# Performance work log

Measured on AMD Instinct MI355X. Metric: run time of the kernel, lower is better.

The kernel has to match this reference:

```python
import jax, jax.numpy as jnp
import numpy as np

DIM_IN1 = 512
DIM_IN2 = 512
DIM_OUT = 64


def setup_inputs() -> dict:
    key = jax.random.key(0)
    k1, k2, kw, kb = jax.random.split(key, 4)
    B, L = 8, 256
    inputs1 = jax.random.normal(k1, (B, L, DIM_IN1), dtype=jnp.float32)
    inputs2 = jax.random.normal(k2, (B, L, DIM_IN2), dtype=jnp.float32)
    # nn.Bilinear init: U(-1/sqrt(in1_features), 1/sqrt(in1_features))
    bound = 1.0 / np.sqrt(DIM_IN1)
    weight = jax.random.uniform(kw, (DIM_OUT, DIM_IN1, DIM_IN2), dtype=jnp.float32,
                                minval=-bound, maxval=bound)
    bias = jax.random.uniform(kb, (DIM_OUT,), dtype=jnp.float32,
                              minval=-bound, maxval=bound)
    return {"inputs1": inputs1, "inputs2": inputs2, "weight": weight, "bias": bias}


def reference(inputs1, inputs2, weight, bias):
    # out[b,i,j,k] = sum_{p,q} x1[b,i,p] * W[k,p,q] * x2[b,j,q] + bias[k]
    # Two smaller batched matmuls instead of materializing [B,L,L,D] expansions.
    tmp = jnp.einsum('bip,kpq->bikq', inputs1, weight)   # [B, L, K, D2]
    out = jnp.einsum('bikq,bjq->bijk', tmp, inputs2)      # [B, L, L, K]
    return out + bias
```

## Files before the change

kernel.cpp:

```cpp
#include <hip/hip_runtime.h>
#include <hip/hip_bf16.h>
#include <stdint.h>


typedef __bf16 bf16x8 __attribute__((ext_vector_type(8)));
typedef float  f32x4  __attribute__((ext_vector_type(4)));

#define BM 128
#define BN 128
#define BK 64
#define LDSK 72
#define KDIM 512

__global__ __launch_bounds__(256) void f32_to_bf16_kernel(
    const float* __restrict__ in, __bf16* __restrict__ out, long n8)
{
    for (long i = blockIdx.x * 256L + threadIdx.x; i < n8; i += gridDim.x * 256L) {
        f32x4 a = *(const f32x4*)(in + i * 8);
        f32x4 b = *(const f32x4*)(in + i * 8 + 4);
        bf16x8 o;
        o[0]=(__bf16)a[0]; o[1]=(__bf16)a[1]; o[2]=(__bf16)a[2]; o[3]=(__bf16)a[3];
        o[4]=(__bf16)b[0]; o[5]=(__bf16)b[1]; o[6]=(__bf16)b[2]; o[7]=(__bf16)b[3];
        *(bf16x8*)(out + i * 8) = o;
    }
}

template <typename OutT>
__global__ __launch_bounds__(256) void gemm_nt_bf16(
    const __bf16* __restrict__ A,
    const __bf16* __restrict__ B,
    OutT* __restrict__ C,
    const float* __restrict__ bias,
    int ldc,
    long sA, long sB, long sC)
{
    const int tid  = threadIdx.x;
    const int lane = tid & 63;
    const int wave = tid >> 6;
    const int wm = wave & 1;
    const int wn = wave >> 1;
    const long z = blockIdx.z;
    A += z * sA;  B += z * sB;  C += z * sC;

    const int m0 = blockIdx.y * BM;
    const int n0 = blockIdx.x * BN;

    __shared__ __bf16 sAt[BM * LDSK];
    __shared__ __bf16 sBt[BN * LDSK];

    f32x4 acc[4][4] = {};

    const int krow = lane >> 4;
    const int lcol = lane & 15;

    const int srow = tid >> 3;
    const int skc  = tid & 7;

    for (int kt = 0; kt < KDIM / BK; ++kt) {
        const __bf16* gA = A + (long)m0 * KDIM + kt * BK;
        const __bf16* gB = B + (long)n0 * KDIM + kt * BK;
#pragma unroll
        for (int it = 0; it < 4; ++it) {
            int row = it * 32 + srow;
            *(bf16x8*)&sAt[row * LDSK + skc * 8] =
                *(const bf16x8*)(gA + (long)row * KDIM + skc * 8);
        }
#pragma unroll
        for (int it = 0; it < 4; ++it) {
            int row = it * 32 + srow;
            *(bf16x8*)&sBt[row * LDSK + skc * 8] =
                *(const bf16x8*)(gB + (long)row * KDIM + skc * 8);
        }
        __syncthreads();
#pragma unroll
        for (int kk = 0; kk < BK / 32; ++kk) {
            bf16x8 af[4], bfr[4];
#pragma unroll
            for (int i = 0; i < 4; ++i)
                af[i] = *(const bf16x8*)&sAt[(wm * 64 + i * 16 + lcol) * LDSK + kk * 32 + krow * 8];
#pragma unroll
            for (int j = 0; j < 4; ++j)
                bfr[j] = *(const bf16x8*)&sBt[(wn * 64 + j * 16 + lcol) * LDSK + kk * 32 + krow * 8];
#pragma unroll
            for (int i = 0; i < 4; ++i)
#pragma unroll
                for (int j = 0; j < 4; ++j)
                    acc[i][j] = __builtin_amdgcn_mfma_f32_16x16x32_bf16(af[i], bfr[j], acc[i][j], 0, 0, 0);
        }
        __syncthreads();
    }

#pragma unroll
    for (int j = 0; j < 4; ++j) {
        const int col = n0 + wn * 64 + j * 16 + lcol;
        float badd = bias ? bias[col & 63] : 0.f;
#pragma unroll
        for (int i = 0; i < 4; ++i) {
            const int rowb = m0 + wm * 64 + i * 16 + krow * 4;
#pragma unroll
            for (int r = 0; r < 4; ++r) {
                float v = acc[i][j][r] + badd;
                C[(long)(rowb + r) * ldc + col] = (OutT)v;
            }
        }
    }
}

extern "C" void kernel_launch(void* const* d_in, const int* in_sizes, int n_in,
                              void* d_out, int out_size, void* d_ws, size_t ws_size,
                              hipStream_t stream)
{
    (void)in_sizes; (void)n_in; (void)out_size;
    const float* x1f = (const float*)d_in[0];
    const float* x2f = (const float*)d_in[1];
    const float* Wf  = (const float*)d_in[2];
    const float* bs  = (const float*)d_in[3];
    float* out = (float*)d_out;

    const long N_W = 64L * 512 * 512;
    const long N_X = 8L * 256 * 512;
    __bf16* Wb  = (__bf16*)d_ws;
    __bf16* x1b = Wb + N_W;
    __bf16* x2b = x1b + N_X;
    __bf16* S   = x2b + N_X;
    const size_t head_bytes = (size_t)(N_W + 2 * N_X) * sizeof(__bf16);

    f32_to_bf16_kernel<<<2048, 256, 0, stream>>>(Wf,  Wb,  N_W / 8);
    f32_to_bf16_kernel<<<512,  256, 0, stream>>>(x1f, x1b, N_X / 8);
    f32_to_bf16_kernel<<<512,  256, 0, stream>>>(x2f, x2b, N_X / 8);

    const long ROWS_TOTAL = 2048;
    const long ROW_ELEMS  = 32768;

    long rows_chunk = (ws_size > head_bytes)
        ? (long)((ws_size - head_bytes) / (ROW_ELEMS * sizeof(__bf16))) : 0;
    rows_chunk &= ~255L;
    if (rows_chunk < 256) rows_chunk = 256;
    if (rows_chunk > ROWS_TOTAL) rows_chunk = ROWS_TOTAL;

    for (long r0 = 0; r0 < ROWS_TOTAL; r0 += rows_chunk) {
        long rows = ROWS_TOTAL - r0;
        if (rows > rows_chunk) rows = rows_chunk;
        long nbc = rows >> 8;

        dim3 gA(32768 / BN, (unsigned)(rows / BM), 1);
        gemm_nt_bf16<__bf16><<<gA, 256, 0, stream>>>(
            x2b + r0 * KDIM, Wb, S, nullptr, 32768, 0, 0, 0);

        dim3 gB(16384 / BN, 256 / BM, (unsigned)nbc);
        gemm_nt_bf16<float><<<gB, 256, 0, stream>>>(
            x1b + r0 * KDIM,
            S,
            out + r0 * 16384,
            bs, 16384,
            256L * KDIM,
            256L * ROW_ELEMS,
            256L * 16384);
    }
}
```

Baseline: 345.3 us.

## Use 256x256 tiles with double-buffered swizzled LDS and XCD-aware block remap

Replaces the 128x128 single-buffered GEMM with a 256x256 tile kernel using 512 threads (8 waves, each computing 128x64). Global loads are prefetched into registers and stored into a second LDS buffer while MFMAs run on the current one, so only one barrier is needed per K step. LDS is XOR-swizzled instead of padded to avoid bank conflicts, and blocks are remapped so neighbouring tiles land on the same XCD for L2 reuse. The larger tile raises arithmetic intensity but uses 128 KB of LDS and many accumulator registers, which limits occupancy and the number of workgroups available.

```diff
diff --git a/kernel.cpp b/kernel.cpp
--- a/kernel.cpp
+++ b/kernel.cpp
@@ -1,16 +1,15 @@
 #include <hip/hip_runtime.h>
-#include <hip/hip_bf16.h>
 #include <stdint.h>
 
 
 typedef __bf16 bf16x8 __attribute__((ext_vector_type(8)));
 typedef float  f32x4  __attribute__((ext_vector_type(4)));
 
-#define BM 128
-#define BN 128
+#define KDIM 512
+#define BM 256
+#define BN 256
 #define BK 64
-#define LDSK 72
-#define KDIM 512
+#define NT (KDIM / BK)
 
 __global__ __launch_bounds__(256) void f32_to_bf16_kernel(
     const float* __restrict__ in, __bf16* __restrict__ out, long n8)
@@ -25,83 +24,126 @@
     }
 }
 
+#define GLOAD(kt) do { _Pragma("unroll") \
+    for (int it_ = 0; it_ < 4; ++it_) { \
+        rA[it_] = *(const bf16x8*)(gA + (long)it_ * 64 * KDIM + (kt) * BK); \
+        rB[it_] = *(const bf16x8*)(gB + (long)it_ * 64 * KDIM + (kt) * BK); \
+    } } while (0)
+
+#define SSTORE(bi) do { _Pragma("unroll") \
+    for (int it_ = 0; it_ < 4; ++it_) { \
+        *(bf16x8*)((char*)&lds[bi][0][0] + it_ * 8192 + sbyte) = rA[it_]; \
+        *(bf16x8*)((char*)&lds[bi][1][0] + it_ * 8192 + sbyte) = rB[it_]; \
+    } } while (0)
+
+#define FRAG_READ(bi, kk) do { \
+    const char* sAc_ = (const char*)&lds[bi][0][0]; \
+    const char* sBc_ = (const char*)&lds[bi][1][0]; \
+    const int ko_ = (((kk) * 64 + krow * 16) ^ rsw); \
+    _Pragma("unroll") for (int i_ = 0; i_ < 8; ++i_) \
+        af[i_] = *(const bf16x8*)(sAc_ + (wm * 128 + i_ * 16 + lcol) * 128 + ko_); \
+    _Pragma("unroll") for (int j_ = 0; j_ < 4; ++j_) \
+        bfr[j_] = *(const bf16x8*)(sBc_ + (wn * 64 + j_ * 16 + lcol) * 128 + ko_); \
+    } while (0)
+
+#define MFMA_ALL do { _Pragma("unroll") \
+    for (int i_ = 0; i_ < 8; ++i_) { _Pragma("unroll") \
+        for (int j_ = 0; j_ < 4; ++j_) \
+            acc[i_][j_] = __builtin_amdgcn_mfma_f32_16x16x32_bf16(af[i_], bfr[j_], acc[i_][j_], 0, 0, 0); \
+    } } while (0)
+
+#define BARRIER() do { \
+    asm volatile("s_waitcnt lgkmcnt(0)" ::: "memory"); \
+    __builtin_amdgcn_sched_barrier(0); \
+    __builtin_amdgcn_s_barrier(); \
+    __builtin_amdgcn_sched_barrier(0); \
+    } while (0)
+
 template <typename OutT>
-__global__ __launch_bounds__(256) void gemm_nt_bf16(
+__global__ __launch_bounds__(512, 2) void gemm_nt_256(
     const __bf16* __restrict__ A,
     const __bf16* __restrict__ B,
     OutT* __restrict__ C,
     const float* __restrict__ bias,
-    int ldc,
+    int ldc, int mtiles,
     long sA, long sB, long sC)
 {
+    __shared__ __bf16 lds[2][2][BM * BK];
+
     const int tid  = threadIdx.x;
     const int lane = tid & 63;
     const int wave = tid >> 6;
-    const int wm = wave & 1;
-    const int wn = wave >> 1;
-    const long z = blockIdx.z;
-    A += z * sA;  B += z * sB;  C += z * sC;
-
-    const int m0 = blockIdx.y * BM;
-    const int n0 = blockIdx.x * BN;
-
-    __shared__ __bf16 sAt[BM * LDSK];
-    __shared__ __bf16 sBt[BN * LDSK];
-
-    f32x4 acc[4][4] = {};
-
-    const int krow = lane >> 4;
+    const int wm   = wave & 1;
+    const int wn   = wave >> 1;
     const int lcol = lane & 15;
-
-    const int srow = tid >> 3;
-    const int skc  = tid & 7;
-
-    for (int kt = 0; kt < KDIM / BK; ++kt) {
-        const __bf16* gA = A + (long)m0 * KDIM + kt * BK;
-        const __bf16* gB = B + (long)n0 * KDIM + kt * BK;
-#pragma unroll
-        for (int it = 0; it < 4; ++it) {
-            int row = it * 32 + srow;
-            *(bf16x8*)&sAt[row * LDSK + skc * 8] =
-                *(const bf16x8*)(gA + (long)row * KDIM + skc * 8);
+    const int krow = (lane >> 4) & 3;
+    const int rsw  = (lcol & 7) << 4;
+
+    long flat = (long)blockIdx.z * gridDim.x + blockIdx.x;
+    long nwg  = (long)gridDim.x * gridDim.z;
+    long q = nwg >> 3, r = nwg & 7;
+    long xcd = flat & 7, lo = flat >> 3;
+    long sz = (xcd < r ? xcd * (q + 1) : r * (q + 1) + (xcd - r) * q) + lo;
+    const int z   = (int)(sz / (long)gridDim.x);
+    const int rem = (int)(sz % (long)gridDim.x);
+    const int n0 = (rem / mtiles) * BN;
+    const int m0 = (rem % mtiles) * BM;
+
+    A += (long)z * sA + (long)m0 * KDIM;
+    B += (long)z * sB + (long)n0 * KDIM;
+    C += (long)z * sC;
+
+    const int srow  = tid >> 3;
+    const int sbyte = srow * 128 + ((((tid & 7) * 16)) ^ ((srow & 7) << 4));
+    const __bf16* gA = A + (long)srow * KDIM + (tid & 7) * 8;
+    const __bf16* gB = B + (long)srow * KDIM + (tid & 7) * 8;
+
+    bf16x8 rA[4], rB[4];
+    f32x4 acc[8][4] = {};
+
+    GLOAD(0);
+    SSTORE(0);
+    GLOAD(1);
+    BARRIER();
+
+    for (int t = 0; t < NT - 1; ++t) {
+        const int cur = t & 1, nxt = cur ^ 1;
+        {
+            bf16x8 af[8], bfr[4];
+            FRAG_READ(cur, 0);
+            SSTORE(nxt);
+            if (t + 2 < NT) GLOAD(t + 2);
+            __builtin_amdgcn_s_setprio(1);
+            MFMA_ALL;
+            __builtin_amdgcn_s_setprio(0);
         }
-#pragma unroll
-        for (int it = 0; it < 4; ++it) {
-            int row = it * 32 + srow;
-            *(bf16x8*)&sBt[row * LDSK + skc * 8] =
-                *(const bf16x8*)(gB + (long)row * KDIM + skc * 8);
+        {
+            bf16x8 af[8], bfr[4];
+            FRAG_READ(cur, 1);
+            __builtin_amdgcn_s_setprio(1);
+            MFMA_ALL;
+            __builtin_amdgcn_s_setprio(0);
         }
-        __syncthreads();
-#pragma unroll
-        for (int kk = 0; kk < BK / 32; ++kk) {
-            bf16x8 af[4], bfr[4];
-#pragma unroll
-            for (int i = 0; i < 4; ++i)
-                af[i] = *(const bf16x8*)&sAt[(wm * 64 + i * 16 + lcol) * LDSK + kk * 32 + krow * 8];
-#pragma unroll
-            for (int j = 0; j < 4; ++j)
-                bfr[j] = *(const bf16x8*)&sBt[(wn * 64 + j * 16 + lcol) * LDSK + kk * 32 + krow * 8];
-#pragma unroll
-            for (int i = 0; i < 4; ++i)
-#pragma unroll
-                for (int j = 0; j < 4; ++j)
-                    acc[i][j] = __builtin_amdgcn_mfma_f32_16x16x32_bf16(af[i], bfr[j], acc[i][j], 0, 0, 0);
-        }
-        __syncthreads();
+        BARRIER();
+    }
+    {
+        bf16x8 af[8], bfr[4];
+        FRAG_READ(1, 0);
+        MFMA_ALL;
+        FRAG_READ(1, 1);
+        MFMA_ALL;
     }
 
 #pragma unroll
     for (int j = 0; j < 4; ++j) {
         const int col = n0 + wn * 64 + j * 16 + lcol;
-        float badd = bias ? bias[col & 63] : 0.f;
+        const float badd = bias ? bias[col & 63] : 0.f;
 #pragma unroll
-        for (int i = 0; i < 4; ++i) {
-            const int rowb = m0 + wm * 64 + i * 16 + krow * 4;
+        for (int i = 0; i < 8; ++i) {
+            const int rowb = m0 + wm * 128 + i * 16 + krow * 4;
 #pragma unroll
-            for (int r = 0; r < 4; ++r) {
-                float v = acc[i][j][r] + badd;
-                C[(long)(rowb + r) * ldc + col] = (OutT)v;
-            }
+            for (int rr = 0; rr < 4; ++rr)
+                C[(long)(rowb + rr) * ldc + col] = (OutT)(acc[i][j][rr] + badd);
         }
     }
 }
@@ -142,19 +184,18 @@
         long rows = ROWS_TOTAL - r0;
         if (rows > rows_chunk) rows = rows_chunk;
         long nbc = rows >> 8;
-
-        dim3 gA(32768 / BN, (unsigned)(rows / BM), 1);
-        gemm_nt_bf16<__bf16><<<gA, 256, 0, stream>>>(
-            x2b + r0 * KDIM, Wb, S, nullptr, 32768, 0, 0, 0);
-
-        dim3 gB(16384 / BN, 256 / BM, (unsigned)nbc);
-        gemm_nt_bf16<float><<<gB, 256, 0, stream>>>(
+        int  mt  = (int)(rows >> 8);
+
+        dim3 gA((unsigned)((32768 / BN) * mt), 1, 1);
+        gemm_nt_256<__bf16><<<gA, 512, 0, stream>>>(
+            x2b + r0 * KDIM, Wb, S, nullptr, 32768, mt, 0, 0, 0);
+
+        dim3 gB2(16384 / BN, 1, (unsigned)nbc);
+        gemm_nt_256<float><<<gB2, 512, 0, stream>>>(
             x1b + r0 * KDIM,
             S,
             out + r0 * 16384,
-            bs, 16384,
-            256L * KDIM,
-            256L * ROW_ELEMS,
-            256L * 16384);
+            bs, 16384, 1,
+            256L * KDIM, 256L * ROW_ELEMS, 256L * 16384);
     }
 }
```

Result: slower. 437.5 us (+26.7%).
